# Optimization experiments

Hardware: AMD Instinct MI355X
Metric: run time of the kernel (lower is better)

Reference implementation:

```python
import jax, jax.numpy as jnp
import numpy as np

# ProjectorConfig defaults
MIN_SPEECH_FRAMES = 1.0
MAX_SPEECH_EXPAND = 3.0
TAIL_HOLD_UNITS = 2
BOUNDARY_COMMIT_THRESHOLD = 0.45

B, U = 4096, 2048


def setup_inputs() -> dict:
    key = jax.random.key(0)
    ks = jax.random.split(key, 10)
    # ragged prefix mask: random visible length per row (faithful to streaming use)
    lengths = jax.random.randint(ks[0], (B,), 1, U + 1)
    unit_mask = (jnp.arange(U)[None, :] < lengths[:, None]).astype(jnp.float32)
    dur_anchor_src = jax.random.uniform(ks[1], (B, U), jnp.float32) * 20.0
    dur_logratio_unit = jax.random.normal(ks[2], (B, U), jnp.float32) * 0.3
    pause_weight_unit = jax.random.uniform(ks[3], (B, U), jnp.float32)
    boundary_latent = jax.random.uniform(ks[4], (B, U), jnp.float32)
    speech_budget_win = jax.random.uniform(ks[5], (B, 1), jnp.float32) * float(U) * 10.0
    pause_budget_win = jax.random.uniform(ks[6], (B, 1), jnp.float32) * float(U)
    open_run_mask = jax.random.bernoulli(ks[7], 0.1, (B, U)).astype(jnp.int32)
    return {
        "dur_anchor_src": dur_anchor_src,
        "unit_mask": unit_mask,
        "speech_budget_win": speech_budget_win,
        "pause_budget_win": pause_budget_win,
        "dur_logratio_unit": dur_logratio_unit,
        "pause_weight_unit": pause_weight_unit,
        "boundary_latent": boundary_latent,
        "phase_ptr": jnp.zeros((B,), jnp.float32),
        "backlog": jnp.zeros((B,), jnp.float32),
        "clock_delta": jnp.zeros((B,), jnp.float32),
        "commit_frontier": jnp.zeros((B,), jnp.int32),
        "open_run_mask": open_run_mask,
    }


def reference(dur_anchor_src, unit_mask, speech_budget_win, pause_budget_win,
              dur_logratio_unit, pause_weight_unit, boundary_latent,
              phase_ptr, backlog, clock_delta, commit_frontier, open_run_mask):
    b, u = unit_mask.shape

    # ---- _project_speech ----
    anchor = jnp.maximum(dur_anchor_src, MIN_SPEECH_FRAMES)
    base = anchor * jnp.exp(dur_logratio_unit)
    speech = jnp.maximum(jnp.minimum(base, anchor * MAX_SPEECH_EXPAND), MIN_SPEECH_FRAMES) * unit_mask
    total = jnp.maximum((speech * unit_mask).sum(axis=1, keepdims=True), 1e-6)
    speech = speech * (speech_budget_win / total) * unit_mask

    # ---- _project_pause ----
    scores = jnp.maximum(pause_weight_unit, 0.0) * (0.5 + boundary_latent) * unit_mask
    score_total = scores.sum(axis=1, keepdims=True)
    fallback = unit_mask / jnp.maximum(unit_mask.sum(axis=1, keepdims=True), 1.0)
    weights = jnp.where(score_total > 0, scores / jnp.maximum(score_total, 1e-6), fallback)
    pause = weights * pause_budget_win

    effective = (speech + pause) * unit_mask

    # ---- _compute_commit_frontier (vectorized) ----
    visible = unit_mask.sum(axis=1).astype(jnp.int32)                 # active_len [B]
    idx = jnp.arange(u, dtype=jnp.int32)[None, :]
    open_vis = (open_run_mask > 0) & (idx < visible[:, None])
    has_open = open_vis.any(axis=1)
    first_open = jnp.argmax(open_vis, axis=1).astype(jnp.int32)
    closed_prefix = jnp.where(has_open, first_open, visible)          # leading closed run
    release_cap = jnp.maximum(visible - TAIL_HOLD_UNITS, 0)
    candidate = jnp.minimum(release_cap, closed_prefix)
    prev = commit_frontier.astype(jnp.int32)
    b_idx = jnp.clip(candidate - 1, 0, u - 1)
    b_val = jnp.take_along_axis(boundary_latent, b_idx[:, None], axis=1)[:, 0]
    soft = (candidate > 0) & (candidate < visible) & (b_val < BOUNDARY_COMMIT_THRESHOLD)
    candidate = jnp.where(soft, jnp.maximum(prev, candidate - 1), candidate)
    commit = jnp.maximum(prev, candidate)

    # ---- _advance_state (prefix sums instead of python loops) ----
    zeros_col = jnp.zeros((b, 1), effective.dtype)
    cs_eff = jnp.concatenate([zeros_col, jnp.cumsum(effective, axis=1)], axis=1)
    cs_src = jnp.concatenate([zeros_col, jnp.cumsum(dur_anchor_src, axis=1)], axis=1)
    take = lambda cs, i: jnp.take_along_axis(cs, i[:, None], axis=1)[:, 0]
    exec_prefix = take(cs_eff, commit) - take(cs_eff, prev)
    src_prefix = take(cs_src, commit) - take(cs_src, prev)
    adv = commit > prev
    delta = exec_prefix - src_prefix
    next_clock = jnp.where(adv, clock_delta + delta, clock_delta)
    next_backlog = jnp.where(adv, jnp.maximum(next_clock, 0.0), backlog)
    visible_total = jnp.maximum(effective.sum(axis=1), 1.0)
    next_phase = jnp.where(adv, jnp.clip(phase_ptr + exec_prefix / visible_total, 0.0, 1.0), phase_ptr)

    return (speech, pause, effective, commit, next_phase, next_backlog, next_clock)
```

## Files before the change

### kernel.cpp

```cpp
#include <hip/hip_runtime.h>
#include <climits>


constexpr int UNITS = 2048;
constexpr int BLOCK = 256;

typedef float f32x4 __attribute__((ext_vector_type(4)));

static __device__ __forceinline__ float waveSum(float v) {
#pragma unroll
  for (int m = 1; m < 64; m <<= 1) v += __shfl_xor(v, m, 64);
  return v;
}

__global__ __launch_bounds__(BLOCK, 8) void rhythm_kernel(
    const float* __restrict__ dur_anchor,
    const float* __restrict__ unit_mask,
    const float* __restrict__ speech_budget,
    const float* __restrict__ pause_budget,
    const float* __restrict__ dur_logratio,
    const float* __restrict__ pause_weight,
    const float* __restrict__ boundary,
    const float* __restrict__ phase_ptr,
    const float* __restrict__ backlog,
    const float* __restrict__ clock_delta,
    const int*   __restrict__ commit_front,
    const int*   __restrict__ open_run,
    float* __restrict__ out,
    int B) {
  const int row = blockIdx.x;
  const int t = threadIdx.x;
  const int wv = t >> 6, ln = t & 63;
  const size_t base = (size_t)row * UNITS;

  const int prev = commit_front[row];
  const float sb = speech_budget[row];
  const float pb = pause_budget[row];

  int visible;
  {
    const int i = (ln < 32) ? ln : 0;
    const float v1 = unit_mask[base + 64 * i + 63];
    const int c1 = __popcll(__ballot((ln < 32) && (v1 > 0.5f)));
    if (c1 == 32) {
      visible = 2048;
    } else {
      const int s = 64 * c1;
      const float v2 = unit_mask[base + s + ln];
      visible = s + __popcll(__ballot(v2 > 0.5f));
    }
  }

  int min_open = INT_MAX;
  for (int cs = 0; cs < visible; cs += 256) {
    const int e = cs + 4 * ln;
    int4 o4 = make_int4(0, 0, 0, 0);
    if (e < visible) o4 = *(const int4*)(open_run + base + e);
    int lm = INT_MAX;
    if (o4.w > 0 && e + 3 < visible) lm = e + 3;
    if (o4.z > 0 && e + 2 < visible) lm = e + 2;
    if (o4.y > 0 && e + 1 < visible) lm = e + 1;
    if (o4.x > 0 && e < visible) lm = e;
    const unsigned long long bb = __ballot(lm != INT_MAX);
    if (bb) {
      min_open = __shfl(lm, (int)__ffsll(bb) - 1, 64);
      break;
    }
  }

  float sv_sr[8];
  float sv_sc[8];
  float sum_sr = 0.f, sum_sc = 0.f;

#pragma unroll
  for (int c = 0; c < 2; ++c) {
    const int e0 = c * 1024 + 4 * t;
    if (e0 < visible) {
      const float4 a4 = *(const float4*)(dur_anchor   + base + e0);
      const float4 l4 = *(const float4*)(dur_logratio + base + e0);
      const float4 p4 = *(const float4*)(pause_weight + base + e0);
      const float4 b4 = *(const float4*)(boundary     + base + e0);
      const float av[4] = {a4.x, a4.y, a4.z, a4.w};
      const float lv[4] = {l4.x, l4.y, l4.z, l4.w};
      const float pv[4] = {p4.x, p4.y, p4.z, p4.w};
      const float bv[4] = {b4.x, b4.y, b4.z, b4.w};
#pragma unroll
      for (int j = 0; j < 4; ++j) {
        const int k = c * 4 + j;
        const float m = (e0 + j < visible) ? 1.0f : 0.0f;
        const float a = fmaxf(av[j], 1.0f);
        const float sr = fmaxf(fminf(a * __expf(lv[j]), 3.0f * a), 1.0f) * m;
        const float sc = fmaxf(pv[j], 0.0f) * (0.5f + bv[j]) * m;
        sv_sr[k] = sr;
        sv_sc[k] = sc;
        sum_sr += sr;
        sum_sc += sc;
      }
    } else {
#pragma unroll
      for (int j = 0; j < 4; ++j) { sv_sr[c * 4 + j] = 0.f; sv_sc[c * 4 + j] = 0.f; }
    }
  }

  __shared__ float sf[2][4];
  const float r0 = waveSum(sum_sr);
  const float r1 = waveSum(sum_sc);
  if (ln == 0) { sf[0][wv] = r0; sf[1][wv] = r1; }
  __syncthreads();

  const float ts = sf[0][0] + sf[0][1] + sf[0][2] + sf[0][3];
  const float tc = sf[1][0] + sf[1][1] + sf[1][2] + sf[1][3];
  const float tm = (float)visible;

  const int closed = (min_open == INT_MAX) ? visible : min_open;
  const int relcap = max(visible - 2, 0);
  int cand = min(relcap, closed);
  const int bidx = min(max(cand - 1, 0), UNITS - 1);
  const float bval = boundary[base + bidx];
  if (cand > 0 && cand < visible && bval < 0.45f)
    cand = max(prev, cand - 1);
  const int commit = max(prev, cand);

  const float sscale = sb / fmaxf(ts, 1e-6f);
  const bool usefb = !(tc > 0.0f);
  const float pscale = pb / fmaxf(tc, 1e-6f);
  const float fbw = pb / fmaxf(tm, 1.0f);
  const float eff_tot = usefb ? (sscale * ts + fbw * tm) : (sscale * ts + pscale * tc);

  float* __restrict__ out_speech = out;
  float* __restrict__ out_pause  = out + (size_t)B * UNITS;
  float* __restrict__ out_eff    = out + 2 * (size_t)B * UNITS;

#pragma unroll
  for (int c = 0; c < 2; ++c) {
    const int e0 = c * 1024 + 4 * t;
    f32x4 s4, q4, e4;
#pragma unroll
    for (int j = 0; j < 4; ++j) {
      const int k = c * 4 + j;
      const float m = (e0 + j < visible) ? 1.0f : 0.0f;
      const float speech = sv_sr[k] * sscale;
      const float pause = usefb ? (m * fbw) : (sv_sc[k] * pscale);
      s4[j] = speech;
      q4[j] = pause;
      e4[j] = speech + pause;
    }
    *(f32x4*)(out_speech + base + e0) = s4;
    *(f32x4*)(out_pause  + base + e0) = q4;
    *(f32x4*)(out_eff    + base + e0) = e4;
  }

  if (wv == 0) {
    float src_rng = 0.f, eff_rng = 0.f;
    if (commit > prev) {
      for (int i = prev + ln; i < commit; i += 64) {
        const float a = dur_anchor[base + i];
        const float l = dur_logratio[base + i];
        const float p = pause_weight[base + i];
        const float bo = boundary[base + i];
        src_rng += a;
        const float aa = fmaxf(a, 1.0f);
        const float sr = fmaxf(fminf(aa * __expf(l), 3.0f * aa), 1.0f);
        const float sc = fmaxf(p, 0.0f) * (0.5f + bo);
        eff_rng += sr * sscale + (usefb ? fbw : sc * pscale);
      }
    }
    const float srcp = waveSum(src_rng);
    const float execp = waveSum(eff_rng);

    if (ln == 0) {
      const float pp = phase_ptr[row];
      const float bl = backlog[row];
      const float cd = clock_delta[row];
      const bool adv = commit > prev;
      const float nclock = adv ? (cd + (execp - srcp)) : cd;
      const float nback = adv ? fmaxf(nclock, 0.0f) : bl;
      const float vt = fmaxf(eff_tot, 1.0f);
      const float nphase =
          adv ? fminf(fmaxf(pp + execp / vt, 0.0f), 1.0f) : pp;
      const size_t o = 3 * (size_t)B * UNITS;
      out[o + row] = (float)commit;
      out[o + (size_t)B + row] = nphase;
      out[o + 2 * (size_t)B + row] = nback;
      out[o + 3 * (size_t)B + row] = nclock;
    }
  }
}

extern "C" void kernel_launch(void* const* d_in, const int* in_sizes, int n_in,
                              void* d_out, int out_size, void* d_ws, size_t ws_size,
                              hipStream_t stream) {
  const int B = in_sizes[7];
  rhythm_kernel<<<dim3(B), dim3(BLOCK), 0, stream>>>(
      (const float*)d_in[0],
      (const float*)d_in[1],
      (const float*)d_in[2],
      (const float*)d_in[3],
      (const float*)d_in[4],
      (const float*)d_in[5],
      (const float*)d_in[6],
      (const float*)d_in[7],
      (const float*)d_in[8],
      (const float*)d_in[9],
      (const int*)d_in[10],
      (const int*)d_in[11],
      (float*)d_out, B);
}
```

Baseline: 246.6 us.

## Process two rows per block and hoist early loads to overlap latency

Each block now handles two rows, row i and row i+B/2, and the grid is halved. The mask probes, first open-run chunks and first data chunk are loaded up front for both rows, so the dependent scalar phase (visible length, open scan, boundary lookup) of the second row overlaps with the first. The first data chunk is now loaded without a visibility guard, so lanes past the visible length read extra memory. The change also raises register pressure and halves the number of blocks, which could reduce occupancy and latency hiding.

```diff
diff --git a/kernel.cpp b/kernel.cpp
--- a/kernel.cpp
+++ b/kernel.cpp
@@ -11,6 +11,142 @@
 #pragma unroll
   for (int m = 1; m < 64; m <<= 1) v += __shfl_xor(v, m, 64);
   return v;
+}
+
+static __device__ __forceinline__ int openScan(const int* __restrict__ open_run,
+                                               size_t base, int ln, int visible,
+                                               int4 o0) {
+  {
+    const int e = 4 * ln;
+    int lm = INT_MAX;
+    if (o0.w > 0 && e + 3 < visible) lm = e + 3;
+    if (o0.z > 0 && e + 2 < visible) lm = e + 2;
+    if (o0.y > 0 && e + 1 < visible) lm = e + 1;
+    if (o0.x > 0 && e < visible)     lm = e;
+    const unsigned long long bb = __ballot(lm != INT_MAX);
+    if (bb) return __shfl(lm, (int)__ffsll(bb) - 1, 64);
+  }
+  for (int cs = 256; cs < visible; cs += 256) {
+    const int e = cs + 4 * ln;
+    int4 o4 = make_int4(0, 0, 0, 0);
+    if (e < visible) o4 = *(const int4*)(open_run + base + e);
+    int lm = INT_MAX;
+    if (o4.w > 0 && e + 3 < visible) lm = e + 3;
+    if (o4.z > 0 && e + 2 < visible) lm = e + 2;
+    if (o4.y > 0 && e + 1 < visible) lm = e + 1;
+    if (o4.x > 0 && e < visible)     lm = e;
+    const unsigned long long bb = __ballot(lm != INT_MAX);
+    if (bb) return __shfl(lm, (int)__ffsll(bb) - 1, 64);
+  }
+  return INT_MAX;
+}
+
+static __device__ __forceinline__ void chunkCompute(
+    const float4& a4, const float4& l4, const float4& p4, const float4& b4,
+    int e, int visible, float* sr_, float* sc_, float& sum_sr, float& sum_sc) {
+  const float av[4] = {a4.x, a4.y, a4.z, a4.w};
+  const float lv[4] = {l4.x, l4.y, l4.z, l4.w};
+  const float pv[4] = {p4.x, p4.y, p4.z, p4.w};
+  const float bv[4] = {b4.x, b4.y, b4.z, b4.w};
+#pragma unroll
+  for (int j = 0; j < 4; ++j) {
+    const float m = (e + j < visible) ? 1.0f : 0.0f;
+    const float a = fmaxf(av[j], 1.0f);
+    const float sr = fmaxf(fminf(a * __expf(lv[j]), 3.0f * a), 1.0f) * m;
+    const float sc = fmaxf(pv[j], 0.0f) * (0.5f + bv[j]) * m;
+    sr_[j] = sr;
+    sc_[j] = sc;
+    sum_sr += sr;
+    sum_sc += sc;
+  }
+}
+
+static __device__ __forceinline__ void finishRow(
+    const float* __restrict__ dur_anchor, const float* __restrict__ dur_logratio,
+    const float* __restrict__ pause_weight, const float* __restrict__ boundary,
+    const float* __restrict__ phase_ptr, const float* __restrict__ backlog,
+    const float* __restrict__ clock_delta, float* __restrict__ out, int B,
+    int row, size_t base, int t, int wv, int ln, int visible, int cand_pre,
+    float bval, int prev, float sb, float pb, const float* sr_,
+    const float* sc_, float sum_sr, float sum_sc, float (*sf)[4]) {
+  const float w0 = waveSum(sum_sr);
+  const float w1 = waveSum(sum_sc);
+  if (ln == 0) { sf[0][wv] = w0; sf[1][wv] = w1; }
+  __syncthreads();
+
+  const float ts = sf[0][0] + sf[0][1] + sf[0][2] + sf[0][3];
+  const float tc = sf[1][0] + sf[1][1] + sf[1][2] + sf[1][3];
+  const float tm = (float)visible;
+
+  int cand = cand_pre;
+  if (cand > 0 && cand < visible && bval < 0.45f)
+    cand = max(prev, cand - 1);
+  const int commit = max(prev, cand);
+
+  const float sscale = sb / fmaxf(ts, 1e-6f);
+  const bool usefb = !(tc > 0.0f);
+  const float pscale = pb / fmaxf(tc, 1e-6f);
+  const float fbw = pb / fmaxf(tm, 1.0f);
+  const float eff_tot = usefb ? (sscale * ts + fbw * tm) : (sscale * ts + pscale * tc);
+
+  float* __restrict__ out_speech = out;
+  float* __restrict__ out_pause  = out + (size_t)B * UNITS;
+  float* __restrict__ out_eff    = out + 2 * (size_t)B * UNITS;
+
+#pragma unroll
+  for (int c = 0; c < 2; ++c) {
+    const int e0 = c * 1024 + 4 * t;
+    f32x4 s4, q4, e4;
+#pragma unroll
+    for (int j = 0; j < 4; ++j) {
+      const int k = c * 4 + j;
+      const float m = (e0 + j < visible) ? 1.0f : 0.0f;
+      const float speech = sr_[k] * sscale;
+      const float pause = usefb ? (m * fbw) : (sc_[k] * pscale);
+      s4[j] = speech;
+      q4[j] = pause;
+      e4[j] = speech + pause;
+    }
+    *(f32x4*)(out_speech + base + e0) = s4;
+    *(f32x4*)(out_pause  + base + e0) = q4;
+    *(f32x4*)(out_eff    + base + e0) = e4;
+  }
+
+  if (wv == 0) {
+    float src_rng = 0.f, eff_rng = 0.f;
+    if (commit > prev) {
+      for (int i = prev + ln; i < commit; i += 64) {
+        const float a = dur_anchor[base + i];
+        const float l = dur_logratio[base + i];
+        const float p = pause_weight[base + i];
+        const float bo = boundary[base + i];
+        src_rng += a;
+        const float aa = fmaxf(a, 1.0f);
+        const float sr = fmaxf(fminf(aa * __expf(l), 3.0f * aa), 1.0f);
+        const float sc = fmaxf(p, 0.0f) * (0.5f + bo);
+        eff_rng += sr * sscale + (usefb ? fbw : sc * pscale);
+      }
+    }
+    const float srcp = waveSum(src_rng);
+    const float execp = waveSum(eff_rng);
+
+    if (ln == 0) {
+      const float pp = phase_ptr[row];
+      const float bl = backlog[row];
+      const float cd = clock_delta[row];
+      const bool adv = commit > prev;
+      const float nclock = adv ? (cd + (execp - srcp)) : cd;
+      const float nback = adv ? fmaxf(nclock, 0.0f) : bl;
+      const float vt = fmaxf(eff_tot, 1.0f);
+      const float nphase =
+          adv ? fminf(fmaxf(pp + execp / vt, 0.0f), 1.0f) : pp;
+      const size_t o = 3 * (size_t)B * UNITS;
+      out[o + row] = (float)commit;
+      out[o + (size_t)B + row] = nphase;
+      out[o + 2 * (size_t)B + row] = nback;
+      out[o + 3 * (size_t)B + row] = nclock;
+    }
+  }
 }
 
 __global__ __launch_bounds__(BLOCK, 8) void rhythm_kernel(
@@ -28,162 +164,112 @@
     const int*   __restrict__ open_run,
     float* __restrict__ out,
     int B) {
-  const int row = blockIdx.x;
+  const int nb = gridDim.x;
+  const int r0 = blockIdx.x;
+  const int r1 = blockIdx.x + nb;
+  const bool has1 = (r1 < B);
   const int t = threadIdx.x;
   const int wv = t >> 6, ln = t & 63;
-  const size_t base = (size_t)row * UNITS;
-
-  const int prev = commit_front[row];
-  const float sb = speech_budget[row];
-  const float pb = pause_budget[row];
-
-  int visible;
+  const size_t base0 = (size_t)r0 * UNITS;
+  const size_t base1 = (size_t)(has1 ? r1 : r0) * UNITS;
+
+  __shared__ float sf0[2][4];
+  __shared__ float sf1[2][4];
+
+  const int pi = 64 * ((ln < 32) ? ln : 0) + 63;
+  const float v1_0 = unit_mask[base0 + pi];
+  const float v1_1 = unit_mask[base1 + pi];
+  const int4 oo0 = *(const int4*)(open_run + base0 + 4 * ln);
+  const int4 oo1 = *(const int4*)(open_run + base1 + 4 * ln);
+  const int e0 = 4 * t;
+  const int e1 = 1024 + 4 * t;
+  const float4 a00 = *(const float4*)(dur_anchor   + base0 + e0);
+  const float4 l00 = *(const float4*)(dur_logratio + base0 + e0);
+  const float4 p00 = *(const float4*)(pause_weight + base0 + e0);
+  const float4 b00 = *(const float4*)(boundary     + base0 + e0);
+
+  const int prev0 = commit_front[r0];
+  const float sb0 = speech_budget[r0], pb0 = pause_budget[r0];
+
+  int visible0, visible1;
   {
-    const int i = (ln < 32) ? ln : 0;
-    const float v1 = unit_mask[base + 64 * i + 63];
-    const int c1 = __popcll(__ballot((ln < 32) && (v1 > 0.5f)));
+    const int c1 = __popcll(__ballot((ln < 32) && (v1_0 > 0.5f)));
     if (c1 == 32) {
-      visible = 2048;
+      visible0 = 2048;
     } else {
       const int s = 64 * c1;
-      const float v2 = unit_mask[base + s + ln];
-      visible = s + __popcll(__ballot(v2 > 0.5f));
-    }
-  }
-
-  int min_open = INT_MAX;
-  for (int cs = 0; cs < visible; cs += 256) {
-    const int e = cs + 4 * ln;
-    int4 o4 = make_int4(0, 0, 0, 0);
-    if (e < visible) o4 = *(const int4*)(open_run + base + e);
-    int lm = INT_MAX;
-    if (o4.w > 0 && e + 3 < visible) lm = e + 3;
-    if (o4.z > 0 && e + 2 < visible) lm = e + 2;
-    if (o4.y > 0 && e + 1 < visible) lm = e + 1;
-    if (o4.x > 0 && e < visible) lm = e;
-    const unsigned long long bb = __ballot(lm != INT_MAX);
-    if (bb) {
-      min_open = __shfl(lm, (int)__ffsll(bb) - 1, 64);
-      break;
-    }
-  }
-
-  float sv_sr[8];
-  float sv_sc[8];
+      const float v2 = unit_mask[base0 + s + ln];
+      visible0 = s + __popcll(__ballot(v2 > 0.5f));
+    }
+  }
+  {
+    const int c1 = __popcll(__ballot((ln < 32) && (v1_1 > 0.5f)));
+    if (c1 == 32) {
+      visible1 = 2048;
+    } else {
+      const int s = 64 * c1;
+      const float v2 = unit_mask[base1 + s + ln];
+      visible1 = s + __popcll(__ballot(v2 > 0.5f));
+    }
+  }
+
+  const int mo0 = openScan(open_run, base0, ln, visible0, oo0);
+  const int mo1 = openScan(open_run, base1, ln, visible1, oo1);
+  const int closed0 = (mo0 == INT_MAX) ? visible0 : mo0;
+  const int closed1 = (mo1 == INT_MAX) ? visible1 : mo1;
+  const int cand0 = min(max(visible0 - 2, 0), closed0);
+  const int cand1 = min(max(visible1 - 2, 0), closed1);
+  const float bval0 = boundary[base0 + min(max(cand0 - 1, 0), UNITS - 1)];
+  const float bval1 = boundary[base1 + min(max(cand1 - 1, 0), UNITS - 1)];
+
+  float sr_[8], sc_[8];
   float sum_sr = 0.f, sum_sc = 0.f;
-
-#pragma unroll
-  for (int c = 0; c < 2; ++c) {
-    const int e0 = c * 1024 + 4 * t;
-    if (e0 < visible) {
-      const float4 a4 = *(const float4*)(dur_anchor   + base + e0);
-      const float4 l4 = *(const float4*)(dur_logratio + base + e0);
-      const float4 p4 = *(const float4*)(pause_weight + base + e0);
-      const float4 b4 = *(const float4*)(boundary     + base + e0);
-      const float av[4] = {a4.x, a4.y, a4.z, a4.w};
-      const float lv[4] = {l4.x, l4.y, l4.z, l4.w};
-      const float pv[4] = {p4.x, p4.y, p4.z, p4.w};
-      const float bv[4] = {b4.x, b4.y, b4.z, b4.w};
-#pragma unroll
-      for (int j = 0; j < 4; ++j) {
-        const int k = c * 4 + j;
-        const float m = (e0 + j < visible) ? 1.0f : 0.0f;
-        const float a = fmaxf(av[j], 1.0f);
-        const float sr = fmaxf(fminf(a * __expf(lv[j]), 3.0f * a), 1.0f) * m;
-        const float sc = fmaxf(pv[j], 0.0f) * (0.5f + bv[j]) * m;
-        sv_sr[k] = sr;
-        sv_sc[k] = sc;
-        sum_sr += sr;
-        sum_sc += sc;
-      }
-    } else {
-#pragma unroll
-      for (int j = 0; j < 4; ++j) { sv_sr[c * 4 + j] = 0.f; sv_sc[c * 4 + j] = 0.f; }
-    }
-  }
-
-  __shared__ float sf[2][4];
-  const float r0 = waveSum(sum_sr);
-  const float r1 = waveSum(sum_sc);
-  if (ln == 0) { sf[0][wv] = r0; sf[1][wv] = r1; }
-  __syncthreads();
-
-  const float ts = sf[0][0] + sf[0][1] + sf[0][2] + sf[0][3];
-  const float tc = sf[1][0] + sf[1][1] + sf[1][2] + sf[1][3];
-  const float tm = (float)visible;
-
-  const int closed = (min_open == INT_MAX) ? visible : min_open;
-  const int relcap = max(visible - 2, 0);
-  int cand = min(relcap, closed);
-  const int bidx = min(max(cand - 1, 0), UNITS - 1);
-  const float bval = boundary[base + bidx];
-  if (cand > 0 && cand < visible && bval < 0.45f)
-    cand = max(prev, cand - 1);
-  const int commit = max(prev, cand);
-
-  const float sscale = sb / fmaxf(ts, 1e-6f);
-  const bool usefb = !(tc > 0.0f);
-  const float pscale = pb / fmaxf(tc, 1e-6f);
-  const float fbw = pb / fmaxf(tm, 1.0f);
-  const float eff_tot = usefb ? (sscale * ts + fbw * tm) : (sscale * ts + pscale * tc);
-
-  float* __restrict__ out_speech = out;
-  float* __restrict__ out_pause  = out + (size_t)B * UNITS;
-  float* __restrict__ out_eff    = out + 2 * (size_t)B * UNITS;
-
-#pragma unroll
-  for (int c = 0; c < 2; ++c) {
-    const int e0 = c * 1024 + 4 * t;
-    f32x4 s4, q4, e4;
-#pragma unroll
-    for (int j = 0; j < 4; ++j) {
-      const int k = c * 4 + j;
-      const float m = (e0 + j < visible) ? 1.0f : 0.0f;
-      const float speech = sv_sr[k] * sscale;
-      const float pause = usefb ? (m * fbw) : (sv_sc[k] * pscale);
-      s4[j] = speech;
-      q4[j] = pause;
-      e4[j] = speech + pause;
-    }
-    *(f32x4*)(out_speech + base + e0) = s4;
-    *(f32x4*)(out_pause  + base + e0) = q4;
-    *(f32x4*)(out_eff    + base + e0) = e4;
-  }
-
-  if (wv == 0) {
-    float src_rng = 0.f, eff_rng = 0.f;
-    if (commit > prev) {
-      for (int i = prev + ln; i < commit; i += 64) {
-        const float a = dur_anchor[base + i];
-        const float l = dur_logratio[base + i];
-        const float p = pause_weight[base + i];
-        const float bo = boundary[base + i];
-        src_rng += a;
-        const float aa = fmaxf(a, 1.0f);
-        const float sr = fmaxf(fminf(aa * __expf(l), 3.0f * aa), 1.0f);
-        const float sc = fmaxf(p, 0.0f) * (0.5f + bo);
-        eff_rng += sr * sscale + (usefb ? fbw : sc * pscale);
-      }
-    }
-    const float srcp = waveSum(src_rng);
-    const float execp = waveSum(eff_rng);
-
-    if (ln == 0) {
-      const float pp = phase_ptr[row];
-      const float bl = backlog[row];
-      const float cd = clock_delta[row];
-      const bool adv = commit > prev;
-      const float nclock = adv ? (cd + (execp - srcp)) : cd;
-      const float nback = adv ? fmaxf(nclock, 0.0f) : bl;
-      const float vt = fmaxf(eff_tot, 1.0f);
-      const float nphase =
-          adv ? fminf(fmaxf(pp + execp / vt, 0.0f), 1.0f) : pp;
-      const size_t o = 3 * (size_t)B * UNITS;
-      out[o + row] = (float)commit;
-      out[o + (size_t)B + row] = nphase;
-      out[o + 2 * (size_t)B + row] = nback;
-      out[o + 3 * (size_t)B + row] = nclock;
-    }
+  chunkCompute(a00, l00, p00, b00, e0, visible0, sr_, sc_, sum_sr, sum_sc);
+  if (e1 < visible0) {
+    const float4 a4 = *(const float4*)(dur_anchor   + base0 + e1);
+    const float4 l4 = *(const float4*)(dur_logratio + base0 + e1);
+    const float4 p4 = *(const float4*)(pause_weight + base0 + e1);
+    const float4 b4 = *(const float4*)(boundary     + base0 + e1);
+    chunkCompute(a4, l4, p4, b4, e1, visible0, sr_ + 4, sc_ + 4, sum_sr, sum_sc);
+  } else {
+#pragma unroll
+    for (int j = 0; j < 4; ++j) { sr_[4 + j] = 0.f; sc_[4 + j] = 0.f; }
+  }
+
+  finishRow(dur_anchor, dur_logratio, pause_weight, boundary, phase_ptr,
+            backlog, clock_delta, out, B, r0, base0, t, wv, ln, visible0,
+            cand0, bval0, prev0, sb0, pb0, sr_, sc_, sum_sr, sum_sc, sf0);
+
+  if (has1) {
+    const int prev1 = commit_front[r1];
+    const float sb1 = speech_budget[r1], pb1 = pause_budget[r1];
+
+    float tr_[8], tc_[8];
+    float s_sr = 0.f, s_sc = 0.f;
+    if (e0 < visible1) {
+      const float4 a4 = *(const float4*)(dur_anchor   + base1 + e0);
+      const float4 l4 = *(const float4*)(dur_logratio + base1 + e0);
+      const float4 p4 = *(const float4*)(pause_weight + base1 + e0);
+      const float4 b4 = *(const float4*)(boundary     + base1 + e0);
+      chunkCompute(a4, l4, p4, b4, e0, visible1, tr_, tc_, s_sr, s_sc);
+    } else {
+#pragma unroll
+      for (int j = 0; j < 4; ++j) { tr_[j] = 0.f; tc_[j] = 0.f; }
+    }
+    if (e1 < visible1) {
+      const float4 a4 = *(const float4*)(dur_anchor   + base1 + e1);
+      const float4 l4 = *(const float4*)(dur_logratio + base1 + e1);
+      const float4 p4 = *(const float4*)(pause_weight + base1 + e1);
+      const float4 b4 = *(const float4*)(boundary     + base1 + e1);
+      chunkCompute(a4, l4, p4, b4, e1, visible1, tr_ + 4, tc_ + 4, s_sr, s_sc);
+    } else {
+#pragma unroll
+      for (int j = 0; j < 4; ++j) { tr_[4 + j] = 0.f; tc_[4 + j] = 0.f; }
+    }
+
+    finishRow(dur_anchor, dur_logratio, pause_weight, boundary, phase_ptr,
+              backlog, clock_delta, out, B, r1, base1, t, wv, ln, visible1,
+              cand1, bval1, prev1, sb1, pb1, tr_, tc_, s_sr, s_sc, sf1);
   }
 }
 
@@ -191,7 +277,8 @@
                               void* d_out, int out_size, void* d_ws, size_t ws_size,
                               hipStream_t stream) {
   const int B = in_sizes[7];
-  rhythm_kernel<<<dim3(B), dim3(BLOCK), 0, stream>>>(
+  const int nb = (B + 1) / 2;
+  rhythm_kernel<<<dim3(nb), dim3(BLOCK), 0, stream>>>(
       (const float*)d_in[0],
       (const float*)d_in[1],
       (const float*)d_in[2],
```

Result: no change. 247.2 us (+0.2%).

## Map one wavefront per row and double-buffer chunk loads

Applied to the files above, without the earlier changes.

Each 64-lane wave now processes a whole row, with four rows per block, instead of one block per row. This removes the shared-memory cross-wave reduction and the __syncthreads, and all waves do the commit-range tail work instead of only wave 0. Loads are double-buffered over eight 256-element chunks, and the boundary value for the commit candidate is fetched early. Per-thread register arrays grow to 64 floats and the launch-bounds occupancy hint drops from 8 to 4, which may lower occupancy and latency hiding.

```diff
diff --git a/kernel.cpp b/kernel.cpp
--- a/kernel.cpp
+++ b/kernel.cpp
@@ -4,6 +4,7 @@
 
 constexpr int UNITS = 2048;
 constexpr int BLOCK = 256;
+constexpr int ROWS_PER_BLOCK = 4;
 
 typedef float f32x4 __attribute__((ext_vector_type(4)));
 
@@ -13,7 +14,7 @@
   return v;
 }
 
-__global__ __launch_bounds__(BLOCK, 8) void rhythm_kernel(
+__global__ __launch_bounds__(BLOCK, 4) void rhythm_kernel(
     const float* __restrict__ dur_anchor,
     const float* __restrict__ unit_mask,
     const float* __restrict__ speech_budget,
@@ -28,9 +29,10 @@
     const int*   __restrict__ open_run,
     float* __restrict__ out,
     int B) {
-  const int row = blockIdx.x;
   const int t = threadIdx.x;
   const int wv = t >> 6, ln = t & 63;
+  const int row = blockIdx.x * ROWS_PER_BLOCK + wv;
+  if (row >= B) return;
   const size_t base = (size_t)row * UNITS;
 
   const int prev = commit_front[row];
@@ -39,8 +41,7 @@
 
   int visible;
   {
-    const int i = (ln < 32) ? ln : 0;
-    const float v1 = unit_mask[base + 64 * i + 63];
+    const float v1 = unit_mask[base + 64 * ((ln < 32) ? ln : 0) + 63];
     const int c1 = __popcll(__ballot((ln < 32) && (v1 > 0.5f)));
     if (c1 == 32) {
       visible = 2048;
@@ -68,57 +69,61 @@
     }
   }
 
-  float sv_sr[8];
-  float sv_sc[8];
+  const int closed = (min_open == INT_MAX) ? visible : min_open;
+  const int cand0 = min(max(visible - 2, 0), closed);
+  const float bval = boundary[base + min(max(cand0 - 1, 0), UNITS - 1)];
+
+  float sr_[8][4];
+  float sc_[8][4];
   float sum_sr = 0.f, sum_sc = 0.f;
 
-#pragma unroll
-  for (int c = 0; c < 2; ++c) {
-    const int e0 = c * 1024 + 4 * t;
-    if (e0 < visible) {
-      const float4 a4 = *(const float4*)(dur_anchor   + base + e0);
-      const float4 l4 = *(const float4*)(dur_logratio + base + e0);
-      const float4 p4 = *(const float4*)(pause_weight + base + e0);
-      const float4 b4 = *(const float4*)(boundary     + base + e0);
-      const float av[4] = {a4.x, a4.y, a4.z, a4.w};
-      const float lv[4] = {l4.x, l4.y, l4.z, l4.w};
-      const float pv[4] = {p4.x, p4.y, p4.z, p4.w};
-      const float bv[4] = {b4.x, b4.y, b4.z, b4.w};
-#pragma unroll
-      for (int j = 0; j < 4; ++j) {
-        const int k = c * 4 + j;
-        const float m = (e0 + j < visible) ? 1.0f : 0.0f;
-        const float a = fmaxf(av[j], 1.0f);
-        const float sr = fmaxf(fminf(a * __expf(lv[j]), 3.0f * a), 1.0f) * m;
-        const float sc = fmaxf(pv[j], 0.0f) * (0.5f + bv[j]) * m;
-        sv_sr[k] = sr;
-        sv_sc[k] = sc;
-        sum_sr += sr;
-        sum_sc += sc;
-      }
-    } else {
-#pragma unroll
-      for (int j = 0; j < 4; ++j) { sv_sr[c * 4 + j] = 0.f; sv_sc[c * 4 + j] = 0.f; }
-    }
-  }
-
-  __shared__ float sf[2][4];
-  const float r0 = waveSum(sum_sr);
-  const float r1 = waveSum(sum_sc);
-  if (ln == 0) { sf[0][wv] = r0; sf[1][wv] = r1; }
-  __syncthreads();
-
-  const float ts = sf[0][0] + sf[0][1] + sf[0][2] + sf[0][3];
-  const float tc = sf[1][0] + sf[1][1] + sf[1][2] + sf[1][3];
+  float4 Ab[2], Lb[2], Pb[2], Bb[2];
+  auto loadChunk = [&](int c, int slot) {
+    const int e = c * 256 + 4 * ln;
+    const float4 z = {0.f, 0.f, 0.f, 0.f};
+    Ab[slot] = z; Lb[slot] = z; Pb[slot] = z; Bb[slot] = z;
+    if (e < visible) {
+      Ab[slot] = *(const float4*)(dur_anchor   + base + e);
+      Lb[slot] = *(const float4*)(dur_logratio + base + e);
+      Pb[slot] = *(const float4*)(pause_weight + base + e);
+      Bb[slot] = *(const float4*)(boundary     + base + e);
+    }
+  };
+
+  loadChunk(0, 0);
+  loadChunk(1, 1);
+#pragma unroll
+  for (int c = 0; c < 8; ++c) {
+    const float4 a4 = Ab[c & 1];
+    const float4 l4 = Lb[c & 1];
+    const float4 p4 = Pb[c & 1];
+    const float4 b4 = Bb[c & 1];
+    if (c + 2 < 8) loadChunk(c + 2, c & 1);
+    const int e = c * 256 + 4 * ln;
+    const float av[4] = {a4.x, a4.y, a4.z, a4.w};
+    const float lv[4] = {l4.x, l4.y, l4.z, l4.w};
+    const float pv[4] = {p4.x, p4.y, p4.z, p4.w};
+    const float bv[4] = {b4.x, b4.y, b4.z, b4.w};
+#pragma unroll
+    for (int j = 0; j < 4; ++j) {
+      const float m = (e + j < visible) ? 1.0f : 0.0f;
+      const float a = fmaxf(av[j], 1.0f);
+      const float sr = fmaxf(fminf(a * __expf(lv[j]), 3.0f * a), 1.0f) * m;
+      const float sc = fmaxf(pv[j], 0.0f) * (0.5f + bv[j]) * m;
+      sr_[c][j] = sr;
+      sc_[c][j] = sc;
+      sum_sr += sr;
+      sum_sc += sc;
+    }
+  }
+
+  const float ts = waveSum(sum_sr);
+  const float tc = waveSum(sum_sc);
   const float tm = (float)visible;
 
-  const int closed = (min_open == INT_MAX) ? visible : min_open;
-  const int relcap = max(visible - 2, 0);
-  int cand = min(relcap, closed);
-  const int bidx = min(max(cand - 1, 0), UNITS - 1);
-  const float bval = boundary[base + bidx];
-  if (cand > 0 && cand < visible && bval < 0.45f)
-    cand = max(prev, cand - 1);
+  int cand = cand0;
+  if (cand0 > 0 && cand0 < visible && bval < 0.45f)
+    cand = max(prev, cand0 - 1);
   const int commit = max(prev, cand);
 
   const float sscale = sb / fmaxf(ts, 1e-6f);
@@ -132,58 +137,55 @@
   float* __restrict__ out_eff    = out + 2 * (size_t)B * UNITS;
 
 #pragma unroll
-  for (int c = 0; c < 2; ++c) {
-    const int e0 = c * 1024 + 4 * t;
+  for (int c = 0; c < 8; ++c) {
+    const int e = c * 256 + 4 * ln;
     f32x4 s4, q4, e4;
 #pragma unroll
     for (int j = 0; j < 4; ++j) {
-      const int k = c * 4 + j;
-      const float m = (e0 + j < visible) ? 1.0f : 0.0f;
-      const float speech = sv_sr[k] * sscale;
-      const float pause = usefb ? (m * fbw) : (sv_sc[k] * pscale);
+      const float m = (e + j < visible) ? 1.0f : 0.0f;
+      const float speech = sr_[c][j] * sscale;
+      const float pause = usefb ? (m * fbw) : (sc_[c][j] * pscale);
       s4[j] = speech;
       q4[j] = pause;
       e4[j] = speech + pause;
     }
-    *(f32x4*)(out_speech + base + e0) = s4;
-    *(f32x4*)(out_pause  + base + e0) = q4;
-    *(f32x4*)(out_eff    + base + e0) = e4;
-  }
-
-  if (wv == 0) {
-    float src_rng = 0.f, eff_rng = 0.f;
-    if (commit > prev) {
-      for (int i = prev + ln; i < commit; i += 64) {
-        const float a = dur_anchor[base + i];
-        const float l = dur_logratio[base + i];
-        const float p = pause_weight[base + i];
-        const float bo = boundary[base + i];
-        src_rng += a;
-        const float aa = fmaxf(a, 1.0f);
-        const float sr = fmaxf(fminf(aa * __expf(l), 3.0f * aa), 1.0f);
-        const float sc = fmaxf(p, 0.0f) * (0.5f + bo);
-        eff_rng += sr * sscale + (usefb ? fbw : sc * pscale);
-      }
-    }
-    const float srcp = waveSum(src_rng);
-    const float execp = waveSum(eff_rng);
-
-    if (ln == 0) {
-      const float pp = phase_ptr[row];
-      const float bl = backlog[row];
-      const float cd = clock_delta[row];
-      const bool adv = commit > prev;
-      const float nclock = adv ? (cd + (execp - srcp)) : cd;
-      const float nback = adv ? fmaxf(nclock, 0.0f) : bl;
-      const float vt = fmaxf(eff_tot, 1.0f);
-      const float nphase =
-          adv ? fminf(fmaxf(pp + execp / vt, 0.0f), 1.0f) : pp;
-      const size_t o = 3 * (size_t)B * UNITS;
-      out[o + row] = (float)commit;
-      out[o + (size_t)B + row] = nphase;
-      out[o + 2 * (size_t)B + row] = nback;
-      out[o + 3 * (size_t)B + row] = nclock;
-    }
+    *(f32x4*)(out_speech + base + e) = s4;
+    *(f32x4*)(out_pause  + base + e) = q4;
+    *(f32x4*)(out_eff    + base + e) = e4;
+  }
+
+  float src_rng = 0.f, eff_rng = 0.f;
+  if (commit > prev) {
+    for (int i = prev + ln; i < commit; i += 64) {
+      const float a = dur_anchor[base + i];
+      const float l = dur_logratio[base + i];
+      const float p = pause_weight[base + i];
+      const float bo = boundary[base + i];
+      src_rng += a;
+      const float aa = fmaxf(a, 1.0f);
+      const float sr = fmaxf(fminf(aa * __expf(l), 3.0f * aa), 1.0f);
+      const float sc = fmaxf(p, 0.0f) * (0.5f + bo);
+      eff_rng += sr * sscale + (usefb ? fbw : sc * pscale);
+    }
+  }
+  const float srcp = waveSum(src_rng);
+  const float execp = waveSum(eff_rng);
+
+  if (ln == 0) {
+    const float pp = phase_ptr[row];
+    const float bl = backlog[row];
+    const float cd = clock_delta[row];
+    const bool adv = commit > prev;
+    const float nclock = adv ? (cd + (execp - srcp)) : cd;
+    const float nback = adv ? fmaxf(nclock, 0.0f) : bl;
+    const float vt = fmaxf(eff_tot, 1.0f);
+    const float nphase =
+        adv ? fminf(fmaxf(pp + execp / vt, 0.0f), 1.0f) : pp;
+    const size_t o = 3 * (size_t)B * UNITS;
+    out[o + row] = (float)commit;
+    out[o + (size_t)B + row] = nphase;
+    out[o + 2 * (size_t)B + row] = nback;
+    out[o + 3 * (size_t)B + row] = nclock;
   }
 }
 
@@ -191,7 +193,8 @@
                               void* d_out, int out_size, void* d_ws, size_t ws_size,
                               hipStream_t stream) {
   const int B = in_sizes[7];
-  rhythm_kernel<<<dim3(B), dim3(BLOCK), 0, stream>>>(
+  const int nb = (B + ROWS_PER_BLOCK - 1) / ROWS_PER_BLOCK;
+  rhythm_kernel<<<dim3(nb), dim3(BLOCK), 0, stream>>>(
       (const float*)d_in[0],
       (const float*)d_in[1],
       (const float*)d_in[2],
```

After: 256.8 us. 4.1% more time.
